# Performance work log

Measured on AMD Instinct MI355X. Metric: run time of the kernel, lower is better.

The kernel has to match this reference:

```python
import jax, jax.numpy as jnp
import numpy as np

N = 20_000_000
B = 16_384


def setup_inputs() -> dict:
    key = jax.random.key(0)
    k1, k2, k3 = jax.random.split(key, 3)
    inp = jax.random.normal(k1, (N,), dtype=jnp.float32)
    tgt = jax.random.normal(k2, (N,), dtype=jnp.float32)
    batch = jnp.sort(jax.random.randint(k3, (N,), 0, B, dtype=jnp.int64))
    return {"input": inp, "target": tgt, "batch": batch, "batch_size": B}


def reference(input, target, batch, batch_size):
    # sum_j c_ij @ c_ij.T over a segment == (segment_sum c)^2
    seg_in = jax.ops.segment_sum(input, batch, num_segments=batch_size)
    seg_tg = jax.ops.segment_sum(target, batch, num_segments=batch_size)
    dot_in = seg_in * seg_in          # [B]
    dot_tg = seg_tg * seg_tg          # [B]
    loss_dot = jnp.sum((dot_in - dot_tg) ** 2)            # F.mse_loss(..., 'sum')
    loss_elem = jnp.sum((jnp.abs(input) - jnp.abs(target)) ** 2)
    return loss_dot + loss_elem
```

## Files before the change

### kernel.cpp

```cpp
#include <hip/hip_runtime.h>

#define BSEG   16384
#define NPART  256
#define LRANGE 64
#define WS_BYTES (2 * BSEG * 4 + NPART * 8)

__global__ __launch_bounds__(256) void main_pass(
        const float* __restrict__ in, const float* __restrict__ tg,
        const int* __restrict__ batch,
        float* __restrict__ seg_in, float* __restrict__ seg_tg,
        double* __restrict__ elem_part, int n)
{
    __shared__ float lsi[LRANGE], lst[LRANGE];
    __shared__ int   firstIdSh;
    __shared__ float wsum[4];

    const int tid  = blockIdx.x * blockDim.x + threadIdx.x;
    const int lane = threadIdx.x & 63;
    const long long i0 = (long long)tid * 8;
    const bool live = (i0 < n);

    float4 a0, a1, t0, t1; int4 c0, c1;
    if (live) {
        const float4* in4 = reinterpret_cast<const float4*>(in + i0);
        const float4* tg4 = reinterpret_cast<const float4*>(tg + i0);
        const int4*   b4  = reinterpret_cast<const int4*>(batch + i0);
        a0 = in4[0]; a1 = in4[1];
        t0 = tg4[0]; t1 = tg4[1];
        c0 = b4[0];  c1 = b4[1];
    }

    for (int k = threadIdx.x; k < LRANGE; k += 256) { lsi[k] = 0.0f; lst[k] = 0.0f; }
    if (threadIdx.x == 0) firstIdSh = c0.x;
    __syncthreads();
    const int firstId = firstIdSh;

    float elem = 0.0f;
    int   cur  = -1;
    float si = 0.0f, st = 0.0f;

    if (live) {
        float vi[8] = {a0.x, a0.y, a0.z, a0.w, a1.x, a1.y, a1.z, a1.w};
        float vt[8] = {t0.x, t0.y, t0.z, t0.w, t1.x, t1.y, t1.z, t1.w};
        int   vb[8] = {c0.x, c0.y, c0.z, c0.w, c1.x, c1.y, c1.z, c1.w};
        cur = vb[0];
        #pragma unroll
        for (int j = 0; j < 8; ++j) {
            float x = vi[j], y = vt[j];
            float d = fabsf(x) - fabsf(y);
            elem = fmaf(d, d, elem);
            int b = vb[j];
            if (b != cur) {
                int off = cur - firstId;
                if (off < LRANGE) { atomicAdd(&lsi[off], si); atomicAdd(&lst[off], st); }
                else { atomicAdd(seg_in + cur, si); atomicAdd(seg_tg + cur, st); }
                cur = b; si = 0.0f; st = 0.0f;
            }
            si += x; st += y;
        }
    }

    #pragma unroll
    for (int d = 1; d < 64; d <<= 1) {
        float o1 = __shfl_up(si, d);
        float o2 = __shfl_up(st, d);
        int  oid = __shfl_up(cur, d);
        if (lane >= d && oid == cur) { si += o1; st += o2; }
    }
    const int  nextId = __shfl_down(cur, 1);
    const bool isTail = (lane == 63) || (nextId != cur);
    if (isTail && cur >= 0) {
        int off = cur - firstId;
        if (off < LRANGE) { atomicAdd(&lsi[off], si); atomicAdd(&lst[off], st); }
        else { atomicAdd(seg_in + cur, si); atomicAdd(seg_tg + cur, st); }
    }

    __syncthreads();
    if (threadIdx.x < LRANGE) {
        float a = lsi[threadIdx.x], b = lst[threadIdx.x];
        if (a != 0.0f || b != 0.0f) {
            atomicAdd(seg_in + firstId + threadIdx.x, a);
            atomicAdd(seg_tg + firstId + threadIdx.x, b);
        }
    }

    #pragma unroll
    for (int off = 32; off; off >>= 1) elem += __shfl_xor(elem, off);
    int wid = threadIdx.x >> 6;
    if (lane == 0) wsum[wid] = elem;
    __syncthreads();
    if (threadIdx.x == 0) {
        float s = wsum[0] + wsum[1] + wsum[2] + wsum[3];
        atomicAdd(elem_part + (blockIdx.x & (NPART - 1)), (double)s);
    }
}

__global__ __launch_bounds__(1024) void finalize_kernel(
        const float* __restrict__ seg_in, const float* __restrict__ seg_tg,
        const double* __restrict__ elem_part, float* __restrict__ out)
{
    const float4* s4 = (const float4*)seg_in;
    const float4* g4 = (const float4*)seg_tg;
    double acc = 0.0;
    for (int i = threadIdx.x; i < BSEG / 4; i += 1024) {
        float4 a = s4[i], b = g4[i];
        float d0 = a.x * a.x - b.x * b.x;
        float d1 = a.y * a.y - b.y * b.y;
        float d2 = a.z * a.z - b.z * b.z;
        float d3 = a.w * a.w - b.w * b.w;
        acc += (double)d0 * d0 + (double)d1 * d1 + (double)d2 * d2 + (double)d3 * d3;
    }
    if (threadIdx.x < NPART) acc += elem_part[threadIdx.x];
    #pragma unroll
    for (int off = 32; off; off >>= 1) acc += __shfl_xor(acc, off);
    __shared__ double wsum[16];
    int lane = threadIdx.x & 63, wid = threadIdx.x >> 6;
    if (lane == 0) wsum[wid] = acc;
    __syncthreads();
    if (threadIdx.x == 0) {
        double t = 0.0;
        #pragma unroll
        for (int w = 0; w < 16; ++w) t += wsum[w];
        out[0] = (float)t;
    }
}

extern "C" void kernel_launch(void* const* d_in, const int* in_sizes, int n_in,
                              void* d_out, int out_size, void* d_ws, size_t ws_size,
                              hipStream_t stream) {
    const float* in    = (const float*)d_in[0];
    const float* tg    = (const float*)d_in[1];
    const int*   batch = (const int*)d_in[2];
    const int n = in_sizes[0];

    float*  seg_in    = (float*)d_ws;
    float*  seg_tg    = seg_in + BSEG;
    double* elem_part = (double*)(seg_in + 2 * BSEG);
    float*  out       = (float*)d_out;

    hipMemsetAsync(d_ws, 0, WS_BYTES, stream);

    const int nthreads = n / 8;
    const int blocks   = (nthreads + 255) / 256;
    main_pass<<<blocks, 256, 0, stream>>>(in, tg, batch, seg_in, seg_tg, elem_part, n);

    finalize_kernel<<<1, 1024, 0, stream>>>(seg_in, seg_tg, elem_part, out);
}
```

Before: 232.9 us.

## Process 16 elements per thread and drop shared-memory segment staging

Each thread now loads 16 elements (four float4/int4 loads per stream) instead of 8, halving the thread count and the per-thread reduction and scan overhead. The shared-memory staging of segment partial sums and the extra block barriers are removed, so partial sums go straight to global atomics. A launch-bounds occupancy hint is added. The trade-off is more global atomics per block, since each warp can span more segments, plus higher register pressure from the larger unrolled chunk.

Result: no change. 231.3 us (-0.7%).

```diff
diff --git a/kernel.cpp b/kernel.cpp
--- a/kernel.cpp
+++ b/kernel.cpp
@@ -2,58 +2,55 @@
 
 #define BSEG   16384
 #define NPART  256
-#define LRANGE 64
+#define CHUNK  16
 #define WS_BYTES (2 * BSEG * 4 + NPART * 8)
 
-__global__ __launch_bounds__(256) void main_pass(
+__global__ __launch_bounds__(256, 4) void main_pass(
         const float* __restrict__ in, const float* __restrict__ tg,
         const int* __restrict__ batch,
         float* __restrict__ seg_in, float* __restrict__ seg_tg,
         double* __restrict__ elem_part, int n)
 {
-    __shared__ float lsi[LRANGE], lst[LRANGE];
-    __shared__ int   firstIdSh;
-    __shared__ float wsum[4];
-
     const int tid  = blockIdx.x * blockDim.x + threadIdx.x;
     const int lane = threadIdx.x & 63;
-    const long long i0 = (long long)tid * 8;
+    const long long i0 = (long long)tid * CHUNK;
     const bool live = (i0 < n);
 
-    float4 a0, a1, t0, t1; int4 c0, c1;
+    float4 a[4], t[4]; int4 c[4];
     if (live) {
         const float4* in4 = reinterpret_cast<const float4*>(in + i0);
         const float4* tg4 = reinterpret_cast<const float4*>(tg + i0);
         const int4*   b4  = reinterpret_cast<const int4*>(batch + i0);
-        a0 = in4[0]; a1 = in4[1];
-        t0 = tg4[0]; t1 = tg4[1];
-        c0 = b4[0];  c1 = b4[1];
+        #pragma unroll
+        for (int q = 0; q < 4; ++q) a[q] = in4[q];
+        #pragma unroll
+        for (int q = 0; q < 4; ++q) t[q] = tg4[q];
+        #pragma unroll
+        for (int q = 0; q < 4; ++q) c[q] = b4[q];
     }
-
-    for (int k = threadIdx.x; k < LRANGE; k += 256) { lsi[k] = 0.0f; lst[k] = 0.0f; }
-    if (threadIdx.x == 0) firstIdSh = c0.x;
-    __syncthreads();
-    const int firstId = firstIdSh;
 
     float elem = 0.0f;
     int   cur  = -1;
     float si = 0.0f, st = 0.0f;
 
     if (live) {
-        float vi[8] = {a0.x, a0.y, a0.z, a0.w, a1.x, a1.y, a1.z, a1.w};
-        float vt[8] = {t0.x, t0.y, t0.z, t0.w, t1.x, t1.y, t1.z, t1.w};
-        int   vb[8] = {c0.x, c0.y, c0.z, c0.w, c1.x, c1.y, c1.z, c1.w};
+        float vi[CHUNK], vt[CHUNK]; int vb[CHUNK];
+        #pragma unroll
+        for (int q = 0; q < 4; ++q) {
+            vi[4*q+0] = a[q].x; vi[4*q+1] = a[q].y; vi[4*q+2] = a[q].z; vi[4*q+3] = a[q].w;
+            vt[4*q+0] = t[q].x; vt[4*q+1] = t[q].y; vt[4*q+2] = t[q].z; vt[4*q+3] = t[q].w;
+            vb[4*q+0] = c[q].x; vb[4*q+1] = c[q].y; vb[4*q+2] = c[q].z; vb[4*q+3] = c[q].w;
+        }
         cur = vb[0];
         #pragma unroll
-        for (int j = 0; j < 8; ++j) {
+        for (int j = 0; j < CHUNK; ++j) {
             float x = vi[j], y = vt[j];
             float d = fabsf(x) - fabsf(y);
             elem = fmaf(d, d, elem);
             int b = vb[j];
             if (b != cur) {
-                int off = cur - firstId;
-                if (off < LRANGE) { atomicAdd(&lsi[off], si); atomicAdd(&lst[off], st); }
-                else { atomicAdd(seg_in + cur, si); atomicAdd(seg_tg + cur, st); }
+                atomicAdd(seg_in + cur, si);
+                atomicAdd(seg_tg + cur, st);
                 cur = b; si = 0.0f; st = 0.0f;
             }
             si += x; st += y;
@@ -70,22 +67,13 @@
     const int  nextId = __shfl_down(cur, 1);
     const bool isTail = (lane == 63) || (nextId != cur);
     if (isTail && cur >= 0) {
-        int off = cur - firstId;
-        if (off < LRANGE) { atomicAdd(&lsi[off], si); atomicAdd(&lst[off], st); }
-        else { atomicAdd(seg_in + cur, si); atomicAdd(seg_tg + cur, st); }
-    }
-
-    __syncthreads();
-    if (threadIdx.x < LRANGE) {
-        float a = lsi[threadIdx.x], b = lst[threadIdx.x];
-        if (a != 0.0f || b != 0.0f) {
-            atomicAdd(seg_in + firstId + threadIdx.x, a);
-            atomicAdd(seg_tg + firstId + threadIdx.x, b);
-        }
+        atomicAdd(seg_in + cur, si);
+        atomicAdd(seg_tg + cur, st);
     }
 
     #pragma unroll
     for (int off = 32; off; off >>= 1) elem += __shfl_xor(elem, off);
+    __shared__ float wsum[4];
     int wid = threadIdx.x >> 6;
     if (lane == 0) wsum[wid] = elem;
     __syncthreads();
@@ -140,7 +128,7 @@
 
     hipMemsetAsync(d_ws, 0, WS_BYTES, stream);
 
-    const int nthreads = n / 8;
+    const int nthreads = n / CHUNK;
     const int blocks   = (nthreads + 255) / 256;
     main_pass<<<blocks, 256, 0, stream>>>(in, tg, batch, seg_in, seg_tg, elem_part, n);
 
```
